# Kernel optimization log

Hardware: AMD Instinct MI355X
Metric: run time of the kernel (lower is better)

Reference implementation:

```python
import jax, jax.numpy as jnp
import numpy as np

N_NODES = 50000
N_EDGES = 800000
IN_DIM = 64
HID_DIM = 64
OUT_DIM = 16
N_RELS = 16
N_BASES = 4


def setup_inputs() -> dict:
    key = jax.random.key(0)
    ks = jax.random.split(key, 11)
    feats = jax.random.normal(ks[0], (N_NODES, IN_DIM), dtype=jnp.float32)
    src = jax.random.randint(ks[1], (N_EDGES,), 0, N_NODES, dtype=jnp.int32)
    dst = jax.random.randint(ks[2], (N_EDGES,), 0, N_NODES, dtype=jnp.int32)
    edge_type = jax.random.randint(ks[3], (N_EDGES,), 0, N_RELS, dtype=jnp.int32)
    edge_norm = jax.random.uniform(ks[4], (N_EDGES,), dtype=jnp.float32)
    # basis-decomposed relation weights: W[r] = sum_b coef[r,b] * bases[b]
    bases1 = jax.random.normal(ks[5], (N_BASES, IN_DIM, HID_DIM), dtype=jnp.float32) * (1.0 / np.sqrt(IN_DIM))
    coef1 = jax.random.normal(ks[6], (N_RELS, N_BASES), dtype=jnp.float32)
    bias1 = jnp.zeros((HID_DIM,), dtype=jnp.float32)
    bases2 = jax.random.normal(ks[7], (N_BASES, HID_DIM, OUT_DIM), dtype=jnp.float32) * (1.0 / np.sqrt(HID_DIM))
    coef2 = jax.random.normal(ks[8], (N_RELS, N_BASES), dtype=jnp.float32)
    bias2 = jnp.zeros((OUT_DIM,), dtype=jnp.float32)
    return {"feats": feats, "src": src, "dst": dst, "edge_type": edge_type,
            "edge_norm": edge_norm, "bases1": bases1, "coef1": coef1, "bias1": bias1,
            "bases2": bases2, "coef2": coef2, "bias2": bias2}


def _rel_graph_conv(x, src, dst, edge_type, edge_norm, bases, coef, bias):
    """One RelGraphConv layer (basis decomposition, low-mem: gather coef, not W)."""
    xs = x[src]                                   # [E, in]  gather source feats
    t = jnp.einsum('ei,bio->ebo', xs, bases)      # [E, B, out] per-basis transform
    c = coef[edge_type]                            # [E, B]   per-edge relation coefs
    msg = jnp.einsum('eb,ebo->eo', c, t)          # [E, out]
    msg = msg * edge_norm[:, None]                # apply edge norm
    h = jax.ops.segment_sum(msg, dst, num_segments=N_NODES)  # scatter-add by dst
    return jax.nn.relu(h + bias)                  # bias + activation (dropout=0, eval)


def reference(feats, src, dst, edge_type, edge_norm, bases1, coef1, bias1, bases2, coef2, bias2):
    h = _rel_graph_conv(feats, src, dst, edge_type, edge_norm, bases1, coef1, bias1)
    h = _rel_graph_conv(h, src, dst, edge_type, edge_norm, bases2, coef2, bias2)
    return h
```

## Files before the change

kernel.cpp:

```cpp
#include <hip/hip_runtime.h>

#define N_NODES 50000
#define N_EDGES 800000

typedef __attribute__((ext_vector_type(8))) short bf16x8;
typedef __attribute__((ext_vector_type(4))) float f32x4;

__device__ __forceinline__ unsigned bf16rne(float x) {
  unsigned u = __float_as_uint(x);
  return (u + 0x7FFFu + ((u >> 16) & 1u)) >> 16;
}
__device__ __forceinline__ unsigned packbf2(float a, float b) {
  return bf16rne(a) | (bf16rne(b) << 16);
}
__device__ __forceinline__ float bflo(unsigned u) { return __uint_as_float(u << 16); }
__device__ __forceinline__ float bfhi(unsigned u) { return __uint_as_float(u & 0xFFFF0000u); }

__global__ __launch_bounds__(256) void k_pack(
    const float4* __restrict__ feats4, uint2* __restrict__ xbf,
    const float* __restrict__ bases1, const float* __restrict__ bases2,
    unsigned short* __restrict__ b1T, unsigned short* __restrict__ b2p) {
  if (blockIdx.x < 3125) {
    const int i = blockIdx.x * 256 + threadIdx.x;
    float4 v = feats4[i];
    xbf[i] = make_uint2(packbf2(v.x, v.y), packbf2(v.z, v.w));
  } else {
    for (int idx = threadIdx.x; idx < 64 * 256; idx += 256) {
      int o = idx >> 8, q = idx & 255;
      b1T[idx] = (unsigned short)bf16rne(bases1[q * 64 + o]);
    }
    for (int idx = threadIdx.x; idx < 64 * 64; idx += 256) {
      int j = idx >> 6, k = idx & 63;
      int o = j >> 2, b = j & 3;
      b2p[idx] = (unsigned short)bf16rne(bases2[b * 1024 + k * 16 + o]);
    }
  }
}

#define G_HIST 64
#define CHUNK (N_EDGES / G_HIST)
#define HPASS 4
#define HBINS (N_NODES / HPASS)

__global__ __launch_bounds__(512) void k_hist(
    const int* __restrict__ dst, int* __restrict__ rank,
    unsigned short* __restrict__ bh) {
  __shared__ int hist[HBINS];
  const int e0 = blockIdx.x * CHUNK;
  unsigned short* bhrow = bh + (size_t)blockIdx.x * N_NODES;
#pragma unroll 1
  for (int p = 0; p < HPASS; ++p) {
    const int lo = p * HBINS;
    for (int i = threadIdx.x; i < HBINS; i += 512) hist[i] = 0;
    __syncthreads();
    for (int i = threadIdx.x; i < CHUNK; i += 512) {
      const int d = dst[e0 + i] - lo;
      if ((unsigned)d < (unsigned)HBINS)
        rank[e0 + i] = atomicAdd(&hist[d], 1);
    }
    __syncthreads();
    for (int i = threadIdx.x; i < HBINS; i += 512)
      bhrow[lo + i] = (unsigned short)hist[i];
    __syncthreads();
  }
}

__global__ __launch_bounds__(1024) void k_scan1(
    unsigned short* __restrict__ bh, int* __restrict__ rowp,
    int* __restrict__ bsum) {
  __shared__ int wsum[16];
  const int tid = threadIdx.x, lane = tid & 63, wid = tid >> 6;
  const int i = blockIdx.x * 1024 + tid;
  int v = 0;
  if (i < N_NODES) {
    int c[G_HIST];
#pragma unroll
    for (int b = 0; b < G_HIST; ++b)
      c[b] = (int)bh[(size_t)b * N_NODES + i];
    int s = 0;
#pragma unroll
    for (int b = 0; b < G_HIST; ++b) {
      const int t = c[b];
      bh[(size_t)b * N_NODES + i] = (unsigned short)s;
      s += t;
    }
    v = s;
  }
  int incl = v;
#pragma unroll
  for (int off = 1; off < 64; off <<= 1) {
    int t = __shfl_up(incl, off, 64);
    if (lane >= off) incl += t;
  }
  if (lane == 63) wsum[wid] = incl;
  __syncthreads();
  if (tid < 16) {
    int wi = wsum[tid];
#pragma unroll
    for (int off = 1; off < 16; off <<= 1) {
      int t = __shfl_up(wi, off, 64);
      if (lane >= off) wi += t;
    }
    wsum[tid] = wi;
  }
  __syncthreads();
  int woff = (wid > 0) ? wsum[wid - 1] : 0;
  int incl_all = incl + woff;
  if (i < N_NODES) rowp[i + 1] = incl_all;
  if (tid == 1023) bsum[blockIdx.x] = incl_all;
}

__global__ __launch_bounds__(1024) void k_scan3(int* __restrict__ rowp,
                                                const int* __restrict__ bsum,
                                                int nblk) {
  __shared__ int s_off;
  const int tid = threadIdx.x;
  if (tid < 64) {
    int v = (tid < nblk && tid < blockIdx.x) ? bsum[tid] : 0;
#pragma unroll
    for (int off = 32; off >= 1; off >>= 1) v += __shfl_down(v, off, 64);
    if (tid == 0) s_off = v;
  }
  __syncthreads();
  const int i = blockIdx.x * 1024 + tid;
  if (i < N_NODES) rowp[i + 1] += s_off;
  if (i == 0) rowp[0] = 0;
}

__global__ __launch_bounds__(256) void k_scatter(
    const int* __restrict__ src, const int* __restrict__ dst,
    const int* __restrict__ ety, const float* __restrict__ enorm,
    const int* __restrict__ rowp, const int* __restrict__ rank,
    const unsigned short* __restrict__ bh, unsigned* __restrict__ s_edge) {
  int e = blockIdx.x * 256 + threadIdx.x;
  if (e >= N_EDGES) return;
  const int d = dst[e];
  const int b = e / CHUNK;
  const int pos = rowp[d] + (int)bh[(size_t)b * N_NODES + d] + rank[e];
  unsigned nq = (unsigned)(enorm[e] * 4096.f + 0.5f);
  nq = nq > 4095u ? 4095u : nq;
  s_edge[pos] = (unsigned)src[e] | ((unsigned)ety[e] << 16) | (nq << 20);
}

#define NMSCALE (1.f / 4096.f)

#define ROWB 264
__device__ __forceinline__ void gather_node(
    const int* __restrict__ rowp, const unsigned* __restrict__ s_edge,
    const uint2* __restrict__ xv, const float4* __restrict__ coefLDS,
    unsigned short* __restrict__ uA,
    int node, int m, int lane) {
  const int eslot = lane >> 4, ch4 = lane & 15;
  const int beg = rowp[node], end = rowp[node + 1];
  float4 a0 = {0, 0, 0, 0}, a1 = {0, 0, 0, 0}, a2 = {0, 0, 0, 0}, a3 = {0, 0, 0, 0};
  int j = beg + eslot;
  unsigned rec0 = 0, rec1 = 0;
  uint2 xp = {0, 0};
  if (j < end) rec0 = s_edge[j];
  if (j + 4 < end) rec1 = s_edge[j + 4];
  if (j < end) xp = xv[(rec0 & 0xFFFF) * 16 + ch4];
  while (j < end) {
    unsigned rec2 = 0;
    uint2 xp1 = {0, 0};
    if (j + 8 < end) rec2 = s_edge[j + 8];
    if (j + 4 < end) xp1 = xv[(rec1 & 0xFFFF) * 16 + ch4];
    const float nm = (float)(rec0 >> 20) * NMSCALE;
    const float4 c = coefLDS[(rec0 >> 16) & 15];
    const float w0 = nm * c.x, w1 = nm * c.y, w2 = nm * c.z, w3 = nm * c.w;
    const float x0 = bflo(xp.x), x1 = bfhi(xp.x), x2 = bflo(xp.y), x3 = bfhi(xp.y);
    a0.x += w0 * x0; a0.y += w0 * x1; a0.z += w0 * x2; a0.w += w0 * x3;
    a1.x += w1 * x0; a1.y += w1 * x1; a1.z += w1 * x2; a1.w += w1 * x3;
    a2.x += w2 * x0; a2.y += w2 * x1; a2.z += w2 * x2; a2.w += w2 * x3;
    a3.x += w3 * x0; a3.y += w3 * x1; a3.z += w3 * x2; a3.w += w3 * x3;
    j += 4; rec0 = rec1; rec1 = rec2; xp = xp1;
  }
#define RED1(x) x += __shfl_down(x, 32, 64)
  RED1(a0.x); RED1(a0.y); RED1(a0.z); RED1(a0.w);
  RED1(a1.x); RED1(a1.y); RED1(a1.z); RED1(a1.w);
  RED1(a2.x); RED1(a2.y); RED1(a2.z); RED1(a2.w);
  RED1(a3.x); RED1(a3.y); RED1(a3.z); RED1(a3.w);
#undef RED1
  if (eslot < 2) {
    unsigned short* row = uA + (eslot * 16 + m) * ROWB + 4 * ch4;
    *(uint2*)(row + 0 * 64) = make_uint2(packbf2(a0.x, a0.y), packbf2(a0.z, a0.w));
    *(uint2*)(row + 1 * 64) = make_uint2(packbf2(a1.x, a1.y), packbf2(a1.z, a1.w));
    *(uint2*)(row + 2 * 64) = make_uint2(packbf2(a2.x, a2.y), packbf2(a2.z, a2.w));
    *(uint2*)(row + 3 * 64) = make_uint2(packbf2(a3.x, a3.y), packbf2(a3.z, a3.w));
  }
}

__global__ __launch_bounds__(256) void k_l1_fused(
    const int* __restrict__ rowp, const unsigned* __restrict__ s_edge,
    const uint2* __restrict__ xbf, const float* __restrict__ coef1,
    const unsigned short* __restrict__ b1T,
    const float* __restrict__ bias1,
    const unsigned short* __restrict__ b2p,
    uint2* __restrict__ y2bf) {
  __shared__ __align__(16) unsigned short uA[2 * 16 * ROWB];
  __shared__ float coefs[64];
  __shared__ float cmat[16 * 68];
  const int wid = threadIdx.x >> 6, lane = threadIdx.x & 63;
  if (threadIdx.x < 64) coefs[threadIdx.x] = coef1[threadIdx.x];
  __syncthreads();
  const int nbase = blockIdx.x * 16;
#pragma unroll
  for (int jn = 0; jn < 4; ++jn) {
    const int m = wid * 4 + jn;
    gather_node(rowp, s_edge, xbf, (const float4*)coefs, uA, nbase + m, m, lane);
  }
  __syncthreads();
  const int nloc = lane & 15, kgrp = lane >> 4;
  f32x4 acc1 = {0.f, 0.f, 0.f, 0.f};
#pragma unroll
  for (int ks = 0; ks < 8; ++ks) {
    const int k0 = ks * 32 + kgrp * 8;
    const bf16x8 b = *(const bf16x8*)&b1T[(wid * 16 + nloc) * 256 + k0];
    const bf16x8 aS0 = *(const bf16x8*)&uA[(0 * 16 + nloc) * ROWB + k0];
    acc1 = __builtin_amdgcn_mfma_f32_16x16x32_bf16(aS0, b, acc1, 0, 0, 0);
    const bf16x8 aS1 = *(const bf16x8*)&uA[(1 * 16 + nloc) * ROWB + k0];
    acc1 = __builtin_amdgcn_mfma_f32_16x16x32_bf16(aS1, b, acc1, 0, 0, 0);
  }
  {
    const int o = wid * 16 + nloc;
    const float bs = bias1[o];
#pragma unroll
    for (int r = 0; r < 4; ++r) {
      const int m = (lane >> 4) * 4 + r;
      cmat[m * 68 + o] = fmaxf(acc1[r] + bs, 0.f);
    }
  }
  __syncthreads();
  f32x4 acc2 = {0.f, 0.f, 0.f, 0.f};
#pragma unroll
  for (int ks = 0; ks < 2; ++ks) {
    const int k0 = ks * 32 + kgrp * 8;
    const float4 c0 = *(const float4*)&cmat[nloc * 68 + k0];
    const float4 c1 = *(const float4*)&cmat[nloc * 68 + k0 + 4];
    union { bf16x8 v; unsigned u[4]; } au;
    au.u[0] = packbf2(c0.x, c0.y); au.u[1] = packbf2(c0.z, c0.w);
    au.u[2] = packbf2(c1.x, c1.y); au.u[3] = packbf2(c1.z, c1.w);
    const bf16x8 b = *(const bf16x8*)&b2p[(wid * 16 + nloc) * 64 + k0];
    acc2 = __builtin_amdgcn_mfma_f32_16x16x32_bf16(au.v, b, acc2, 0, 0, 0);
  }
  __syncthreads();
#pragma unroll
  for (int r = 0; r < 4; ++r) {
    const int m = (lane >> 4) * 4 + r;
    cmat[m * 68 + wid * 16 + nloc] = acc2[r];
  }
  __syncthreads();
  const int nl = threadIdx.x >> 4, c4 = threadIdx.x & 15;
  const float* cr = &cmat[nl * 68 + 4 * c4];
  y2bf[(size_t)(nbase + nl) * 16 + c4] =
      make_uint2(packbf2(cr[0], cr[1]), packbf2(cr[2], cr[3]));
}

__global__ __launch_bounds__(256) void k_l2_gather(
    const int* __restrict__ rowp, const unsigned* __restrict__ s_edge,
    const uint4* __restrict__ y2v,
    const float* __restrict__ coef2, const float* __restrict__ bias2,
    float2* __restrict__ out) {
  __shared__ float coefs[64];
  if (threadIdx.x < 64) coefs[threadIdx.x] = coef2[threadIdx.x];
  __syncthreads();
  const float4* coefv = (const float4*)coefs;
  const int wid = threadIdx.x >> 6, lane = threadIdx.x & 63;
  const int eslot = lane >> 3, og = lane & 7;
  const int nbase = blockIdx.x * 8 + wid * 2;

  int j[2], jend[2];
  float a0[2] = {0.f, 0.f}, a1[2] = {0.f, 0.f};
  unsigned r0[2], r1[2];
  uint4 yp[2];
#pragma unroll
  for (int m = 0; m < 2; ++m) {
    const int node = nbase + m;
    const int beg = rowp[node];
    jend[m] = rowp[node + 1];
    j[m] = beg + eslot;
    r0[m] = 0; r1[m] = 0;
    yp[m] = make_uint4(0, 0, 0, 0);
    if (j[m] < jend[m]) r0[m] = s_edge[j[m]];
    if (j[m] + 8 < jend[m]) r1[m] = s_edge[j[m] + 8];
  }
#pragma unroll
  for (int m = 0; m < 2; ++m)
    if (j[m] < jend[m]) yp[m] = y2v[(r0[m] & 0xFFFF) * 8 + og];

  while ((j[0] < jend[0]) | (j[1] < jend[1])) {
#pragma unroll
    for (int m = 0; m < 2; ++m) {
      unsigned r2 = 0;
      uint4 yp1 = make_uint4(0, 0, 0, 0);
      if (j[m] + 16 < jend[m]) r2 = s_edge[j[m] + 16];
      if (j[m] + 8 < jend[m]) yp1 = y2v[(r1[m] & 0xFFFF) * 8 + og];
      if (j[m] < jend[m]) {
        const float nm = (float)(r0[m] >> 20) * NMSCALE;
        const float4 c = coefv[(r0[m] >> 16) & 15];
        a0[m] += nm * (c.x * bflo(yp[m].x) + c.y * bfhi(yp[m].x) +
                       c.z * bflo(yp[m].y) + c.w * bfhi(yp[m].y));
        a1[m] += nm * (c.x * bflo(yp[m].z) + c.y * bfhi(yp[m].z) +
                       c.z * bflo(yp[m].w) + c.w * bfhi(yp[m].w));
      }
      j[m] += 8; r0[m] = r1[m]; r1[m] = r2; yp[m] = yp1;
    }
  }
#pragma unroll
  for (int m = 0; m < 2; ++m) {
    a0[m] += __shfl_down(a0[m], 32, 64);
    a0[m] += __shfl_down(a0[m], 16, 64);
    a0[m] += __shfl_down(a0[m], 8, 64);
    a1[m] += __shfl_down(a1[m], 32, 64);
    a1[m] += __shfl_down(a1[m], 16, 64);
    a1[m] += __shfl_down(a1[m], 8, 64);
  }
  if (eslot == 0) {
    const float b0 = bias2[2 * og], b1 = bias2[2 * og + 1];
#pragma unroll
    for (int m = 0; m < 2; ++m) {
      out[(size_t)(nbase + m) * 8 + og] =
          make_float2(fmaxf(a0[m] + b0, 0.f), fmaxf(a1[m] + b1, 0.f));
    }
  }
}

extern "C" void kernel_launch(void* const* d_in, const int* in_sizes, int n_in,
                              void* d_out, int out_size, void* d_ws, size_t ws_size,
                              hipStream_t stream) {
  const float* feats  = (const float*)d_in[0];
  const int*   src    = (const int*)d_in[1];
  const int*   dst    = (const int*)d_in[2];
  const int*   etype  = (const int*)d_in[3];
  const float* enorm  = (const float*)d_in[4];
  const float* bases1 = (const float*)d_in[5];
  const float* coef1  = (const float*)d_in[6];
  const float* bias1  = (const float*)d_in[7];
  const float* bases2 = (const float*)d_in[8];
  const float* coef2  = (const float*)d_in[9];
  const float* bias2  = (const float*)d_in[10];

  uint2* xbf    = (uint2*)d_ws;
  uint2* y2bf   = xbf + (size_t)N_NODES * 16;
  unsigned* s_edge = (unsigned*)(y2bf + (size_t)N_NODES * 16);
  int*   rank   = (int*)(s_edge + N_EDGES);
  unsigned short* bh = (unsigned short*)(rank + N_EDGES);
  unsigned short* b1T = bh + (size_t)G_HIST * N_NODES;
  unsigned short* b2p = b1T + 64 * 256;
  int*   rowp   = (int*)(b2p + 64 * 64);
  int*   bsum   = rowp + N_NODES + 1;

  const int SCAN_BLKS = (N_NODES + 1023) / 1024;

  k_pack<<<3126, 256, 0, stream>>>((const float4*)feats, xbf, bases1,
                                   bases2, b1T, b2p);
  k_hist<<<G_HIST, 512, 0, stream>>>(dst, rank, bh);
  k_scan1<<<SCAN_BLKS, 1024, 0, stream>>>(bh, rowp, bsum);
  k_scan3<<<SCAN_BLKS, 1024, 0, stream>>>(rowp, bsum, SCAN_BLKS);
  k_scatter<<<N_EDGES / 256, 256, 0, stream>>>(src, dst, etype, enorm,
                                               rowp, rank, bh, s_edge);
  k_l1_fused<<<N_NODES / 16, 256, 0, stream>>>(rowp, s_edge, xbf, coef1,
                                               b1T, bias1, b2p, y2bf);
  k_l2_gather<<<N_NODES / 8, 256, 0, stream>>>(rowp, s_edge,
                                               (const uint4*)y2bf, coef2,
                                               bias2, (float2*)d_out);
}
```

Baseline: 209.4 us.

## Shrink histogram block count and transpose per-block offset table to node-major

The edge-count histogram now uses 16 edge chunks instead of 64, and the per-block count table is stored node-major (node × chunk) instead of chunk-major. The scan kernel can then read and write each node's 16 counts as two contiguous 16-byte vectors, and the scatter kernel's offset lookup touches one small contiguous row per destination. This shrinks the offset table and the scan's memory traffic. In exchange, only 16 blocks build the histogram, each doing four times more serial LDS-atomic work, and the histogram write-out becomes strided 2-byte stores.

New measurement: 299.2 us. 42.9% more time.

```diff
diff --git a/kernel.cpp b/kernel.cpp
--- a/kernel.cpp
+++ b/kernel.cpp
@@ -37,7 +37,7 @@
   }
 }
 
-#define G_HIST 64
+#define G_HIST 16
 #define CHUNK (N_EDGES / G_HIST)
 #define HPASS 4
 #define HBINS (N_NODES / HPASS)
@@ -47,7 +47,6 @@
     unsigned short* __restrict__ bh) {
   __shared__ int hist[HBINS];
   const int e0 = blockIdx.x * CHUNK;
-  unsigned short* bhrow = bh + (size_t)blockIdx.x * N_NODES;
 #pragma unroll 1
   for (int p = 0; p < HPASS; ++p) {
     const int lo = p * HBINS;
@@ -60,30 +59,33 @@
     }
     __syncthreads();
     for (int i = threadIdx.x; i < HBINS; i += 512)
-      bhrow[lo + i] = (unsigned short)hist[i];
+      bh[(size_t)(lo + i) * G_HIST + blockIdx.x] = (unsigned short)hist[i];
     __syncthreads();
   }
 }
 
 __global__ __launch_bounds__(1024) void k_scan1(
-    unsigned short* __restrict__ bh, int* __restrict__ rowp,
-    int* __restrict__ bsum) {
+    uint4* __restrict__ bh4,
+    int* __restrict__ rowp, int* __restrict__ bsum) {
   __shared__ int wsum[16];
   const int tid = threadIdx.x, lane = tid & 63, wid = tid >> 6;
   const int i = blockIdx.x * 1024 + tid;
   int v = 0;
   if (i < N_NODES) {
-    int c[G_HIST];
-#pragma unroll
-    for (int b = 0; b < G_HIST; ++b)
-      c[b] = (int)bh[(size_t)b * N_NODES + i];
+    uint4 u0 = bh4[(size_t)i * 2 + 0];
+    uint4 u1 = bh4[(size_t)i * 2 + 1];
+    unsigned w[8] = {u0.x, u0.y, u0.z, u0.w, u1.x, u1.y, u1.z, u1.w};
+    unsigned o[8];
     int s = 0;
 #pragma unroll
-    for (int b = 0; b < G_HIST; ++b) {
-      const int t = c[b];
-      bh[(size_t)b * N_NODES + i] = (unsigned short)s;
-      s += t;
-    }
+    for (int k = 0; k < 8; ++k) {
+      const int clo = (int)(w[k] & 0xFFFFu), chi = (int)(w[k] >> 16);
+      const unsigned plo = (unsigned)s; s += clo;
+      const unsigned phi = (unsigned)s; s += chi;
+      o[k] = plo | (phi << 16);
+    }
+    bh4[(size_t)i * 2 + 0] = make_uint4(o[0], o[1], o[2], o[3]);
+    bh4[(size_t)i * 2 + 1] = make_uint4(o[4], o[5], o[6], o[7]);
     v = s;
   }
   int incl = v;
@@ -136,7 +138,7 @@
   if (e >= N_EDGES) return;
   const int d = dst[e];
   const int b = e / CHUNK;
-  const int pos = rowp[d] + (int)bh[(size_t)b * N_NODES + d] + rank[e];
+  const int pos = rowp[d] + (int)bh[(size_t)d * G_HIST + b] + rank[e];
   unsigned nq = (unsigned)(enorm[e] * 4096.f + 0.5f);
   nq = nq > 4095u ? 4095u : nq;
   s_edge[pos] = (unsigned)src[e] | ((unsigned)ety[e] << 16) | (nq << 20);
@@ -344,7 +346,7 @@
   unsigned* s_edge = (unsigned*)(y2bf + (size_t)N_NODES * 16);
   int*   rank   = (int*)(s_edge + N_EDGES);
   unsigned short* bh = (unsigned short*)(rank + N_EDGES);
-  unsigned short* b1T = bh + (size_t)G_HIST * N_NODES;
+  unsigned short* b1T = bh + (size_t)N_NODES * G_HIST;
   unsigned short* b2p = b1T + 64 * 256;
   int*   rowp   = (int*)(b2p + 64 * 64);
   int*   bsum   = rowp + N_NODES + 1;
@@ -354,7 +356,7 @@
   k_pack<<<3126, 256, 0, stream>>>((const float4*)feats, xbf, bases1,
                                    bases2, b1T, b2p);
   k_hist<<<G_HIST, 512, 0, stream>>>(dst, rank, bh);
-  k_scan1<<<SCAN_BLKS, 1024, 0, stream>>>(bh, rowp, bsum);
+  k_scan1<<<SCAN_BLKS, 1024, 0, stream>>>((uint4*)bh, rowp, bsum);
   k_scan3<<<SCAN_BLKS, 1024, 0, stream>>>(rowp, bsum, SCAN_BLKS);
   k_scatter<<<N_EDGES / 256, 256, 0, stream>>>(src, dst, etype, enorm,
                                                rowp, rank, bh, s_edge);
```

## Parallelize histogram passes across blocks and tile the scan through shared memory

Applied to the files above, without the earlier changes.

The histogram kernel used to run its four destination-range passes one after another inside each of 64 blocks. It now launches 256 blocks, one per (chunk, slice) pair, so all slices run at the same time and more CUs are occupied. The per-node scan over the 64 chunk counts now loads a 64x512 tile of ushort counts into shared memory with vectorized uint2 accesses, replacing strided per-thread global reads and writes. The scan block size drops to 512, which gives about 98 scan blocks, so scan3 now loops over bsum instead of assuming at most 64 blocks. Each histogram block still reads its whole edge chunk, so global reads of dst grow fourfold in exchange for the extra parallelism.

After: 191.1 us. 1.1x faster.

```diff
diff --git a/kernel.cpp b/kernel.cpp
--- a/kernel.cpp
+++ b/kernel.cpp
@@ -39,53 +39,61 @@
 
 #define G_HIST 64
 #define CHUNK (N_EDGES / G_HIST)
-#define HPASS 4
-#define HBINS (N_NODES / HPASS)
+#define NSLICE 4
+#define HBINS (N_NODES / NSLICE)
 
 __global__ __launch_bounds__(512) void k_hist(
     const int* __restrict__ dst, int* __restrict__ rank,
     unsigned short* __restrict__ bh) {
   __shared__ int hist[HBINS];
-  const int e0 = blockIdx.x * CHUNK;
-  unsigned short* bhrow = bh + (size_t)blockIdx.x * N_NODES;
-#pragma unroll 1
-  for (int p = 0; p < HPASS; ++p) {
-    const int lo = p * HBINS;
-    for (int i = threadIdx.x; i < HBINS; i += 512) hist[i] = 0;
-    __syncthreads();
-    for (int i = threadIdx.x; i < CHUNK; i += 512) {
-      const int d = dst[e0 + i] - lo;
-      if ((unsigned)d < (unsigned)HBINS)
-        rank[e0 + i] = atomicAdd(&hist[d], 1);
-    }
-    __syncthreads();
-    for (int i = threadIdx.x; i < HBINS; i += 512)
-      bhrow[lo + i] = (unsigned short)hist[i];
-    __syncthreads();
-  }
-}
-
-__global__ __launch_bounds__(1024) void k_scan1(
-    unsigned short* __restrict__ bh, int* __restrict__ rowp,
-    int* __restrict__ bsum) {
-  __shared__ int wsum[16];
-  const int tid = threadIdx.x, lane = tid & 63, wid = tid >> 6;
-  const int i = blockIdx.x * 1024 + tid;
-  int v = 0;
-  if (i < N_NODES) {
-    int c[G_HIST];
-#pragma unroll
-    for (int b = 0; b < G_HIST; ++b)
-      c[b] = (int)bh[(size_t)b * N_NODES + i];
-    int s = 0;
-#pragma unroll
-    for (int b = 0; b < G_HIST; ++b) {
-      const int t = c[b];
-      bh[(size_t)b * N_NODES + i] = (unsigned short)s;
-      s += t;
-    }
-    v = s;
-  }
+  const int c = blockIdx.x & (G_HIST - 1);
+  const int p = blockIdx.x >> 6;
+  const int e0 = c * CHUNK;
+  const int lo = p * HBINS;
+  for (int i = threadIdx.x; i < HBINS; i += 512) hist[i] = 0;
+  __syncthreads();
+  for (int i = threadIdx.x; i < CHUNK; i += 512) {
+    const int d = dst[e0 + i] - lo;
+    if ((unsigned)d < (unsigned)HBINS)
+      rank[e0 + i] = atomicAdd(&hist[d], 1);
+  }
+  __syncthreads();
+  for (int i = threadIdx.x; i < HBINS; i += 512)
+    bh[(size_t)c * N_NODES + lo + i] = (unsigned short)hist[i];
+}
+
+#define NB 512
+__global__ __launch_bounds__(512) void k_scan1(
+    unsigned short* __restrict__ bh,
+    int* __restrict__ rowp, int* __restrict__ bsum) {
+  __shared__ unsigned short tile[G_HIST][NB];
+  __shared__ int wsum[8];
+  const int tid = threadIdx.x;
+  const int n0 = blockIdx.x * NB;
+  for (int idx = tid; idx < G_HIST * (NB / 4); idx += 512) {
+    const int c = idx >> 7, j = idx & 127;
+    const int nloc = 4 * j;
+    uint2 u = make_uint2(0u, 0u);
+    if (n0 + nloc < N_NODES)
+      u = *(const uint2*)(bh + (size_t)c * N_NODES + n0 + nloc);
+    *(uint2*)&tile[c][nloc] = u;
+  }
+  __syncthreads();
+  int s = 0;
+  for (int c = 0; c < G_HIST; ++c) {
+    const int cnt = tile[c][tid];
+    tile[c][tid] = (unsigned short)s;
+    s += cnt;
+  }
+  __syncthreads();
+  for (int idx = tid; idx < G_HIST * (NB / 4); idx += 512) {
+    const int c = idx >> 7, j = idx & 127;
+    const int nloc = 4 * j;
+    if (n0 + nloc < N_NODES)
+      *(uint2*)(bh + (size_t)c * N_NODES + n0 + nloc) = *(uint2*)&tile[c][nloc];
+  }
+  const int lane = tid & 63, wid = tid >> 6;
+  int v = (n0 + tid < N_NODES) ? s : 0;
   int incl = v;
 #pragma unroll
   for (int off = 1; off < 64; off <<= 1) {
@@ -94,10 +102,10 @@
   }
   if (lane == 63) wsum[wid] = incl;
   __syncthreads();
-  if (tid < 16) {
+  if (tid < 8) {
     int wi = wsum[tid];
 #pragma unroll
-    for (int off = 1; off < 16; off <<= 1) {
+    for (int off = 1; off < 8; off <<= 1) {
       int t = __shfl_up(wi, off, 64);
       if (lane >= off) wi += t;
     }
@@ -106,23 +114,23 @@
   __syncthreads();
   int woff = (wid > 0) ? wsum[wid - 1] : 0;
   int incl_all = incl + woff;
-  if (i < N_NODES) rowp[i + 1] = incl_all;
-  if (tid == 1023) bsum[blockIdx.x] = incl_all;
-}
-
-__global__ __launch_bounds__(1024) void k_scan3(int* __restrict__ rowp,
-                                                const int* __restrict__ bsum,
-                                                int nblk) {
+  if (n0 + tid < N_NODES) rowp[n0 + tid + 1] = incl_all;
+  if (tid == NB - 1) bsum[blockIdx.x] = incl_all;
+}
+
+__global__ __launch_bounds__(512) void k_scan3(int* __restrict__ rowp,
+                                               const int* __restrict__ bsum) {
   __shared__ int s_off;
   const int tid = threadIdx.x;
   if (tid < 64) {
-    int v = (tid < nblk && tid < blockIdx.x) ? bsum[tid] : 0;
+    int v = 0;
+    for (int b = tid; b < (int)blockIdx.x; b += 64) v += bsum[b];
 #pragma unroll
     for (int off = 32; off >= 1; off >>= 1) v += __shfl_down(v, off, 64);
     if (tid == 0) s_off = v;
   }
   __syncthreads();
-  const int i = blockIdx.x * 1024 + tid;
+  const int i = blockIdx.x * NB + tid;
   if (i < N_NODES) rowp[i + 1] += s_off;
   if (i == 0) rowp[0] = 0;
 }
@@ -349,13 +357,13 @@
   int*   rowp   = (int*)(b2p + 64 * 64);
   int*   bsum   = rowp + N_NODES + 1;
 
-  const int SCAN_BLKS = (N_NODES + 1023) / 1024;
+  const int SCAN_BLKS = (N_NODES + NB - 1) / NB;
 
   k_pack<<<3126, 256, 0, stream>>>((const float4*)feats, xbf, bases1,
                                    bases2, b1T, b2p);
-  k_hist<<<G_HIST, 512, 0, stream>>>(dst, rank, bh);
-  k_scan1<<<SCAN_BLKS, 1024, 0, stream>>>(bh, rowp, bsum);
-  k_scan3<<<SCAN_BLKS, 1024, 0, stream>>>(rowp, bsum, SCAN_BLKS);
+  k_hist<<<G_HIST * NSLICE, 512, 0, stream>>>(dst, rank, bh);
+  k_scan1<<<SCAN_BLKS, 512, 0, stream>>>(bh, rowp, bsum);
+  k_scan3<<<SCAN_BLKS, 512, 0, stream>>>(rowp, bsum);
   k_scatter<<<N_EDGES / 256, 256, 0, stream>>>(src, dst, etype, enorm,
                                                rowp, rank, bh, s_edge);
   k_l1_fused<<<N_NODES / 16, 256, 0, stream>>>(rowp, s_edge, xbf, coef1,
```
